# Performance work log

Measured on AMD Instinct MI355X. Metric: run time of the kernel, lower is better.

The kernel has to match this reference:

```python
import jax, jax.numpy as jnp
import numpy as np

B, S, D, H = 4, 1024, 1024, 16
HS = D // H  # head_size = 64


def setup_inputs() -> dict:
    key = jax.random.key(0)
    ks = jax.random.split(key, 12)
    sc_d = 1.0 / np.sqrt(D)
    sc_h = 1.0 / np.sqrt(HS)
    inp = {
        "queries": jax.random.normal(ks[0], (B, S, D), jnp.float32),
        "keys": jax.random.normal(ks[1], (B, S, D), jnp.float32),
        "values": jax.random.normal(ks[2], (B, S, D), jnp.float32),
        # causal mask: scores where mask == 0 are filled with -1e9
        "mask": jnp.tril(jnp.ones((S, S), jnp.int32)),
        # per-head query/key projections: [H, D, HS] weights, [H, HS] biases
        "Wq": jax.random.uniform(ks[3], (H, D, HS), jnp.float32, -sc_d, sc_d),
        "bq": jax.random.uniform(ks[4], (H, HS), jnp.float32, -sc_d, sc_d),
        "Wk": jax.random.uniform(ks[5], (H, D, HS), jnp.float32, -sc_d, sc_d),
        "bk": jax.random.uniform(ks[6], (H, HS), jnp.float32, -sc_d, sc_d),
        # shared value projection: [D, HS]
        "Wv": jax.random.uniform(ks[7], (D, HS), jnp.float32, -sc_d, sc_d),
        "bv": jax.random.uniform(ks[8], (HS,), jnp.float32, -sc_d, sc_d),
        # output projection: [HS, D]
        "Wo": jax.random.uniform(ks[9], (HS, D), jnp.float32, -sc_h, sc_h),
        "bo": jax.random.uniform(ks[10], (D,), jnp.float32, -sc_h, sc_h),
    }
    return inp


def reference(queries, keys, values, mask, Wq, bq, Wk, bk, Wv, bv, Wo, bo):
    # shared value projection: [B, S, HS]
    v = jnp.einsum("bsd,de->bse", values, Wv) + bv
    # batched per-head projections (replaces the python loop over heads)
    q = jnp.einsum("bsd,hde->bhse", queries, Wq) + bq[None, :, None, :]
    k = jnp.einsum("btd,hde->bhte", keys, Wk) + bk[None, :, None, :]
    scores = jnp.einsum("bhse,bhte->bhst", q, k) / jnp.sqrt(jnp.float32(HS))
    scores = jnp.where(mask == 0, jnp.float32(-1e9), scores)
    attn = jax.nn.softmax(scores, axis=-1)  # [B, H, S, S]; dropout = eval-mode identity
    head_out = jnp.einsum("bhst,bte->bhse", attn, v)
    out = head_out.mean(axis=1)  # mean over heads -> [B, S, HS]
    out = jnp.einsum("bse,ed->bsd", out, Wo) + bo
    attention_weights = attn.mean(axis=1)  # [B, S, S]
    return out, attention_weights
```

## Files before the change

### kernel.cpp

```cpp
#include <hip/hip_runtime.h>
#include <hip/hip_bf16.h>
#include <stdint.h>

typedef _Float16 half8 __attribute__((ext_vector_type(8)));
typedef _Float16 half4 __attribute__((ext_vector_type(4)));
typedef float    f32x4 __attribute__((ext_vector_type(4)));

#define MFMA16(a, b, c) __builtin_amdgcn_mfma_f32_16x16x32_f16(a, b, c, 0, 0, 0)

typedef __attribute__((address_space(1))) const void GVOID;
typedef __attribute__((address_space(3))) void LVOID;
__device__ __forceinline__ void glds16(const void* g, void* l)
{
    __builtin_amdgcn_global_load_lds((GVOID*)g, (LVOID*)l, 16, 0, 0);
}

__global__ __launch_bounds__(256) void transpose_to_f16(
    const float* __restrict__ X, _Float16* __restrict__ Y,
    int R, int C, long inBS, long outBS)
{
    __shared__ float t[32][33];
    const int bz = blockIdx.z;
    X += (long)bz * inBS;
    Y += (long)bz * outBS;
    const int c0 = blockIdx.x * 32, r0 = blockIdx.y * 32;
    const int tx = threadIdx.x & 31, ty = threadIdx.x >> 5;
#pragma unroll
    for (int i = 0; i < 4; ++i)
        t[ty + i * 8][tx] = X[(long)(r0 + ty + i * 8) * C + c0 + tx];
    __syncthreads();
#pragma unroll
    for (int i = 0; i < 4; ++i)
        Y[(long)(c0 + ty + i * 8) * R + r0 + tx] = (_Float16)t[tx][ty + i * 8];
}

__global__ __launch_bounds__(256) void cvt_qk_f16(
    const float* __restrict__ S0, const float* __restrict__ S1,
    _Float16* __restrict__ D)
{
    const float* S = blockIdx.y ? S1 : S0;
    _Float16* Dz = D + (long)blockIdx.y * 4194304;
    const long i = ((long)blockIdx.x * 256 + threadIdx.x) * 8;
    const float4 v0 = *(const float4*)(S + i);
    const float4 v1 = *(const float4*)(S + i + 4);
    half8 h;
    h[0] = (_Float16)v0.x; h[1] = (_Float16)v0.y;
    h[2] = (_Float16)v0.z; h[3] = (_Float16)v0.w;
    h[4] = (_Float16)v1.x; h[5] = (_Float16)v1.y;
    h[6] = (_Float16)v1.z; h[7] = (_Float16)v1.w;
    *(half8*)(Dz + i) = h;
}

__global__ __launch_bounds__(256, 2) void gemm_qk_glds(
    const _Float16* __restrict__ A16,
    const _Float16* __restrict__ BT,
    const float* __restrict__ bias0, const float* __restrict__ bias1,
    _Float16* __restrict__ Cout)
{
    __shared__ __align__(16) _Float16 As[2][128 * 64];
    __shared__ __align__(16) _Float16 Bs[2][128 * 64];

    const int gx  = gridDim.x, gy = gridDim.y;
    const int nwg = gx * gy * (int)gridDim.z;
    const int lid = (int)blockIdx.x + gx * ((int)blockIdx.y + gy * (int)blockIdx.z);
    const int q8  = nwg >> 3;
    const int xcd = lid & 7, loc = lid >> 3;
    const int sw  = xcd * q8 + loc;
    const int nt  = sw % gx;
    const int tm2 = sw / gx;
    const int mt  = tm2 % gy;
    const int z   = tm2 / gy;

    const int n0 = nt * 128;
    const int m0 = mt * 128;
    const int tid  = threadIdx.x;
    const int wave = tid >> 6, lane = tid & 63;
    const int m16  = lane & 15, quad = lane >> 4;

    const char* Az = (const char*)(A16 + (long)z * 4194304);
    const char* Bz = (const char*)(BT  + (long)z * 1048576);

    const int colbyte = (((lane & 7) ^ (lane >> 3)) << 4);
    const char* gaBase = Az + ((long)(m0 + wave * 32 + (lane >> 3)) << 11) + colbyte;
    const char* gbBase = Bz + ((long)(n0 + wave * 32 + (lane >> 3)) << 11) + colbyte;

    f32x4 acc[2][8];
    {
        f32x4 zz = {0.f, 0.f, 0.f, 0.f};
#pragma unroll
        for (int i = 0; i < 2; ++i)
#pragma unroll
            for (int j = 0; j < 8; ++j) acc[i][j] = zz;
    }

    auto STAGE = [&](int bf, int k0) {
        const char* ga = gaBase + (k0 << 1);
        const char* gb = gbBase + (k0 << 1);
        _Float16* la = &As[bf][wave * 32 * 64];
        _Float16* lb = &Bs[bf][wave * 32 * 64];
#pragma unroll
        for (int i = 0; i < 4; ++i) {
            glds16(ga + (long)i * 8 * 2048, la + i * 8 * 64);
            glds16(gb + (long)i * 8 * 2048, lb + i * 8 * 64);
        }
    };

    auto COMPUTE = [&](int bf) {
        const char* Ab = (const char*)&As[bf][0];
        const char* Bp = (const char*)&Bs[bf][0];
        const int sw4 = (m16 & 7) << 4;
#pragma unroll
        for (int kss = 0; kss < 2; ++kss) {
            const int kbs = (kss * 64 + quad * 16) ^ sw4;
            const half8 a0 = *(const half8*)(Ab + (wave * 32 + m16) * 128 + kbs);
            const half8 a1 = *(const half8*)(Ab + (wave * 32 + 16 + m16) * 128 + kbs);
#pragma unroll
            for (int c = 0; c < 8; ++c) {
                const half8 bfr = *(const half8*)(Bp + (c * 16 + m16) * 128 + kbs);
                acc[0][c] = MFMA16(a0, bfr, acc[0][c]);
                acc[1][c] = MFMA16(a1, bfr, acc[1][c]);
            }
        }
    };

    STAGE(0, 0);
    __syncthreads();
    int cur = 0;
    for (int k0 = 0; k0 < 1024; k0 += 64) {
        if (k0 + 64 < 1024) STAGE(cur ^ 1, k0 + 64);
        COMPUTE(cur);
        __syncthreads();
        cur ^= 1;
    }

    const float* bias = z ? bias1 : bias0;
    _Float16* Cz = Cout + (long)z * 4194304;
#pragma unroll
    for (int hh = 0; hh < 2; ++hh) {
#pragma unroll
        for (int c = 0; c < 8; ++c) {
            const int col = n0 + c * 16 + m16;
            const float bb = bias[col];
#pragma unroll
            for (int r = 0; r < 4; ++r) {
                const int row = m0 + wave * 32 + hh * 16 + quad * 4 + r;
                Cz[(long)row * 1024 + col] = (_Float16)(acc[hh][c][r] + bb);
            }
        }
    }
}

__global__ __launch_bounds__(256, 2) void gemm_f16_v2(
    const float* __restrict__ A0, const float* __restrict__ A1,
    const _Float16* __restrict__ BT,
    const float* __restrict__ bias0, const float* __restrict__ bias1,
    void* __restrict__ Cout,
    int N, int lda, int ldbt, int ldc,
    long aBS, long bBS, long cBS,
    int c_half, int atomic, int nks, int kchunk)
{
    __shared__ __align__(16) _Float16 As[128][72];
    __shared__ __align__(16) _Float16 Bs[128][72];

    const int gx  = gridDim.x, gy = gridDim.y;
    const int nwg = gx * gy * (int)gridDim.z;
    const int lid = (int)blockIdx.x + gx * ((int)blockIdx.y + gy * (int)blockIdx.z);
    const int q8  = nwg >> 3, r8 = nwg & 7;
    const int xcd = lid & 7, loc = lid >> 3;
    const int sw  = (xcd < r8 ? xcd * (q8 + 1) : r8 * (q8 + 1) + (xcd - r8) * q8) + loc;
    const int nt  = sw % gx;
    const int tm2 = sw / gx;
    const int mt  = tm2 % gy;
    const int bz  = tm2 / gy;

    const int b = bz / nks, ks = bz % nks;
    const int kbeg = ks * kchunk;
    const int kend = kbeg + kchunk;

    const float* A = A1 ? (b ? A1 : A0) : (A0 + (long)b * aBS);
    const _Float16* Bb = BT + (long)b * bBS;

    const int n0 = nt * 128;
    const int m0 = mt * 128;
    const int tid  = threadIdx.x;
    const int wave = tid >> 6, lane = tid & 63;
    const int m16  = lane & 15, quad = lane >> 4;

    const int acol = (tid & 15) * 4;
    const int arb  = tid >> 4;
    const int bj   = tid >> 1;
    const int bcc  = (tid & 1) * 32;
    int jn = n0 + bj; if (jn > N - 1) jn = N - 1;
    const _Float16* bpB = Bb + (long)jn * ldbt;

    f32x4 acc[2][8];
    {
        f32x4 zz = {0.f, 0.f, 0.f, 0.f};
#pragma unroll
        for (int i = 0; i < 2; ++i)
#pragma unroll
            for (int j = 0; j < 8; ++j) acc[i][j] = zz;
    }

    for (int k0 = kbeg; k0 < kend; k0 += 64) {
        {
            const int cc = acol;
            float4 av[8];
#pragma unroll
            for (int p = 0; p < 8; ++p)
                av[p] = *(const float4*)(A + (long)(m0 + arb + p * 16) * lda + k0 + cc);
#pragma unroll
            for (int p = 0; p < 8; ++p) {
                half4 hv;
                hv[0] = (_Float16)av[p].x; hv[1] = (_Float16)av[p].y;
                hv[2] = (_Float16)av[p].z; hv[3] = (_Float16)av[p].w;
                *(half4*)&As[arb + p * 16][cc] = hv;
            }
        }
        {
            const _Float16* bp = bpB + k0 + bcc;
            half8 b0 = *(const half8*)(bp);
            half8 b1 = *(const half8*)(bp + 8);
            half8 b2 = *(const half8*)(bp + 16);
            half8 b3 = *(const half8*)(bp + 24);
            *(half8*)&Bs[bj][bcc]      = b0;
            *(half8*)&Bs[bj][bcc + 8]  = b1;
            *(half8*)&Bs[bj][bcc + 16] = b2;
            *(half8*)&Bs[bj][bcc + 24] = b3;
        }
        __syncthreads();
#pragma unroll
        for (int kss = 0; kss < 2; ++kss) {
            const int ko = kss * 32 + quad * 8;
            const half8 a0 = *(const half8*)&As[wave * 32 + m16][ko];
            const half8 a1 = *(const half8*)&As[wave * 32 + 16 + m16][ko];
#pragma unroll
            for (int c = 0; c < 8; ++c) {
                const half8 bf = *(const half8*)&Bs[c * 16 + m16][ko];
                acc[0][c] = MFMA16(a0, bf, acc[0][c]);
                acc[1][c] = MFMA16(a1, bf, acc[1][c]);
            }
        }
        __syncthreads();
    }

    const float* bias = b ? bias1 : bias0;
    const int addb = (bias != nullptr) && (kbeg == 0);
#pragma unroll
    for (int hh = 0; hh < 2; ++hh) {
#pragma unroll
        for (int c = 0; c < 8; ++c) {
            const int col = n0 + c * 16 + m16;
            if (col >= N) continue;
            const float bb = addb ? bias[col] : 0.f;
#pragma unroll
            for (int r = 0; r < 4; ++r) {
                const int row = m0 + wave * 32 + hh * 16 + quad * 4 + r;
                const float v = acc[hh][c][r] + bb;
                const long idx = (long)b * cBS + (long)row * ldc + col;
                if (atomic)      atomicAdd(&((float*)Cout)[idx], v);
                else if (c_half) ((_Float16*)Cout)[idx] = (_Float16)v;
                else             ((float*)Cout)[idx] = v;
            }
        }
    }
}

__global__ __launch_bounds__(256, 4) void attn_stats(
    const _Float16* __restrict__ q_all, const _Float16* __restrict__ k_all,
    float* __restrict__ m_out, float* __restrict__ il_out)
{
    const int st = blockIdx.x, h = blockIdx.y, b = blockIdx.z;
    const int tid = threadIdx.x, wave = tid >> 6, lane = tid & 63;
    const int m16 = lane & 15, quad = lane >> 4;
    const int s0 = st * 64;
    const int sw = s0 + wave * 16;

    __shared__ __align__(16) _Float16 qs[64][72];
    __shared__ __align__(16) _Float16 ks[64][72];

    const int srow = tid >> 2;
    const int scol = (tid & 3) * 16;

    {
        const _Float16* qsrc = q_all + ((long)(b * 1024 + s0 + srow)) * 1024 + h * 64 + scol;
        *(half8*)&qs[srow][scol]     = *(const half8*)(qsrc);
        *(half8*)&qs[srow][scol + 8] = *(const half8*)(qsrc + 8);
    }

    const _Float16* ksrcb = k_all + ((long)(b * 1024 + srow)) * 1024 + h * 64 + scol;

    float mr[4], lr[4];
#pragma unroll
    for (int r = 0; r < 4; ++r) { mr[r] = -3.0e38f; lr[r] = 0.f; }

    half8 a0, a1;
    for (int tt = 0; tt <= st; ++tt) {
        const _Float16* ksrc = ksrcb + (long)(tt * 64) * 1024;
        const half8 k0 = *(const half8*)(ksrc);
        const half8 k1 = *(const half8*)(ksrc + 8);

        __syncthreads();
        *(half8*)&ks[srow][scol]     = k0;
        *(half8*)&ks[srow][scol + 8] = k1;
        __syncthreads();

        if (tt == 0) {
            a0 = *(const half8*)&qs[wave * 16 + m16][quad * 8];
            a1 = *(const half8*)&qs[wave * 16 + m16][quad * 8 + 32];
        }

        if (tt < st) {
#pragma unroll
            for (int c = 0; c < 4; ++c) {
                const half8 b0 = *(const half8*)&ks[c * 16 + m16][quad * 8];
                const half8 b1 = *(const half8*)&ks[c * 16 + m16][quad * 8 + 32];
                f32x4 cc = {0.f, 0.f, 0.f, 0.f};
                cc = MFMA16(a0, b0, cc);
                cc = MFMA16(a1, b1, cc);
#pragma unroll
                for (int r = 0; r < 4; ++r) {
                    const float zz = cc[r] * 0.125f;
                    const float nm = fmaxf(mr[r], zz);
                    lr[r] = lr[r] * __expf(mr[r] - nm) + __expf(zz - nm);
                    mr[r] = nm;
                }
            }
        } else {
#pragma unroll
            for (int c = 0; c < 4; ++c) {
                const half8 b0 = *(const half8*)&ks[c * 16 + m16][quad * 8];
                const half8 b1 = *(const half8*)&ks[c * 16 + m16][quad * 8 + 32];
                f32x4 cc = {0.f, 0.f, 0.f, 0.f};
                cc = MFMA16(a0, b0, cc);
                cc = MFMA16(a1, b1, cc);
                const int col = tt * 64 + c * 16 + m16;
#pragma unroll
                for (int r = 0; r < 4; ++r) {
                    const int row = sw + quad * 4 + r;
                    if (col <= row) {
                        const float zz = cc[r] * 0.125f;
                        const float nm = fmaxf(mr[r], zz);
                        lr[r] = lr[r] * __expf(mr[r] - nm) + __expf(zz - nm);
                        mr[r] = nm;
                    }
                }
            }
        }
    }

#pragma unroll
    for (int mk = 1; mk < 16; mk <<= 1) {
#pragma unroll
        for (int r = 0; r < 4; ++r) {
            const float om = __shfl_xor(mr[r], mk);
            const float ol = __shfl_xor(lr[r], mk);
            const float nm = fmaxf(mr[r], om);
            lr[r] = lr[r] * __expf(mr[r] - nm) + ol * __expf(om - nm);
            mr[r] = nm;
        }
    }
    if (m16 == 0) {
#pragma unroll
        for (int r = 0; r < 4; ++r) {
            const long idx = ((long)(b * 16 + h)) * 1024 + sw + quad * 4 + r;
            m_out[idx]  = mr[r];
            il_out[idx] = 1.f / lr[r];
        }
    }
}

__global__ __launch_bounds__(256, 4) void attn_pmean(
    const _Float16* __restrict__ q_all, const _Float16* __restrict__ k_all,
    const float* __restrict__ m_in, const float* __restrict__ il_in,
    const _Float16* __restrict__ vT,
    float* __restrict__ attn,
    float* __restrict__ ctx)
{
    const int ttile = blockIdx.x, stile = blockIdx.y, b = blockIdx.z;
    const int tid = threadIdx.x;
    if (ttile > stile) {
        const int c4 = (tid & 15) * 4;
        float4 zz = {0.f, 0.f, 0.f, 0.f};
#pragma unroll
        for (int i = 0; i < 4; ++i) {
            const int r = stile * 64 + (tid >> 4) + i * 16;
            *(float4*)&attn[((long)(b * 1024 + r)) * 1024 + ttile * 64 + c4] = zz;
        }
        return;
    }

    __shared__ __align__(16) _Float16 qs[64][72];
    __shared__ __align__(16) _Float16 ks[64][72];
    __shared__ __align__(16) _Float16 ps[64][72];

    const int wave = tid >> 6, lane = tid & 63;
    const int m16 = lane & 15, quad = lane >> 4;
    const int s0 = stile * 64;
    const int t0 = ttile * 64;
    const int sw = s0 + wave * 16;
    const int diag = (ttile == stile);

    const int srow = tid >> 2;
    const int scol = (tid & 3) * 16;

    const _Float16* qsrc = q_all + ((long)(b * 1024 + s0 + srow)) * 1024 + scol;
    const _Float16* ksrc = k_all + ((long)(b * 1024 + t0 + srow)) * 1024 + scol;
    const long sbase = ((long)(b * 16)) * 1024 + sw + quad * 4;

    float pm[4][4];
#pragma unroll
    for (int c = 0; c < 4; ++c)
#pragma unroll
        for (int r = 0; r < 4; ++r) pm[c][r] = 0.f;

    for (int h = 0; h < 16; ++h) {
        const int ho = h * 64;
        const half8 q0 = *(const half8*)(qsrc + ho);
        const half8 q1 = *(const half8*)(qsrc + ho + 8);
        const half8 k0 = *(const half8*)(ksrc + ho);
        const half8 k1 = *(const half8*)(ksrc + ho + 8);
        const long idx = sbase + (long)h * 1024;
        const float4 mv = *(const float4*)&m_in[idx];
        const float4 iv = *(const float4*)&il_in[idx];

        __syncthreads();
        *(half8*)&qs[srow][scol]     = q0;
        *(half8*)&qs[srow][scol + 8] = q1;
        *(half8*)&ks[srow][scol]     = k0;
        *(half8*)&ks[srow][scol + 8] = k1;
        __syncthreads();

        const half8 a0 = *(const half8*)&qs[wave * 16 + m16][quad * 8];
        const half8 a1 = *(const half8*)&qs[wave * 16 + m16][quad * 8 + 32];
        const float mrow[4] = {mv.x, mv.y, mv.z, mv.w};
        const float irow[4] = {iv.x, iv.y, iv.z, iv.w};

        if (!diag) {
#pragma unroll
            for (int c = 0; c < 4; ++c) {
                const half8 b0 = *(const half8*)&ks[c * 16 + m16][quad * 8];
                const half8 b1 = *(const half8*)&ks[c * 16 + m16][quad * 8 + 32];
                f32x4 cc = {0.f, 0.f, 0.f, 0.f};
                cc = MFMA16(a0, b0, cc);
                cc = MFMA16(a1, b1, cc);
#pragma unroll
                for (int r = 0; r < 4; ++r)
                    pm[c][r] += __expf(cc[r] * 0.125f - mrow[r]) * irow[r];
            }
        } else {
#pragma unroll
            for (int c = 0; c < 4; ++c) {
                const half8 b0 = *(const half8*)&ks[c * 16 + m16][quad * 8];
                const half8 b1 = *(const half8*)&ks[c * 16 + m16][quad * 8 + 32];
                f32x4 cc = {0.f, 0.f, 0.f, 0.f};
                cc = MFMA16(a0, b0, cc);
                cc = MFMA16(a1, b1, cc);
                const int col = t0 + c * 16 + m16;
#pragma unroll
                for (int r = 0; r < 4; ++r) {
                    const int row = sw + quad * 4 + r;
                    if (col <= row)
                        pm[c][r] += __expf(cc[r] * 0.125f - mrow[r]) * irow[r];
                }
            }
        }
    }

#pragma unroll
    for (int c = 0; c < 4; ++c) {
#pragma unroll
        for (int r = 0; r < 4; ++r) {
            const int rloc = (wave << 4) + (quad << 2) + r;
            const int cloc = c * 16 + m16;
            const float p = pm[c][r] * 0.0625f;
            attn[((long)(b * 1024 + s0 + rloc)) * 1024 + t0 + cloc] = p;
            ps[rloc][cloc] = (_Float16)p;
        }
    }
    __syncthreads();

    const _Float16* vTb = vT + (long)b * 65536 + t0;
    f32x4 apv[4];
    {
        f32x4 zz = {0.f, 0.f, 0.f, 0.f};
#pragma unroll
        for (int c = 0; c < 4; ++c) apv[c] = zz;
    }
#pragma unroll
    for (int kss = 0; kss < 2; ++kss) {
        const half8 a = *(const half8*)&ps[wave * 16 + m16][kss * 32 + quad * 8];
#pragma unroll
        for (int c = 0; c < 4; ++c) {
            const half8 bf = *(const half8*)(vTb + (long)(c * 16 + m16) * 1024 + kss * 32 + quad * 8);
            apv[c] = MFMA16(a, bf, apv[c]);
        }
    }
#pragma unroll
    for (int c = 0; c < 4; ++c) {
#pragma unroll
        for (int r = 0; r < 4; ++r) {
            const int row = sw + quad * 4 + r;
            const int e   = c * 16 + m16;
            atomicAdd(&ctx[((long)(b * 1024 + row)) * 64 + e], apv[c][r]);
        }
    }
}

extern "C" void kernel_launch(void* const* d_in, const int* in_sizes, int n_in,
                              void* d_out, int out_size, void* d_ws, size_t ws_size,
                              hipStream_t stream)
{
    const float* queries = (const float*)d_in[0];
    const float* keys    = (const float*)d_in[1];
    const float* values  = (const float*)d_in[2];
    const float* Wq = (const float*)d_in[4];
    const float* bq = (const float*)d_in[5];
    const float* Wk = (const float*)d_in[6];
    const float* bk = (const float*)d_in[7];
    const float* Wv = (const float*)d_in[8];
    const float* bv = (const float*)d_in[9];
    const float* Wo = (const float*)d_in[10];
    const float* bo = (const float*)d_in[11];

    float* out_ptr  = (float*)d_out;
    float* attn_ptr = out_ptr + (long)4096 * 1024;

    uint8_t* w = (uint8_t*)d_ws;
    size_t off = 0;
    auto alloc = [&](size_t bytes) {
        void* p = w + off;
        off = (off + bytes + 255) & ~(size_t)255;
        return p;
    };
    _Float16* WqkT  = (_Float16*)alloc((size_t)2 * 1024 * 1024 * 2);
    _Float16* WvT   = (_Float16*)alloc((size_t)64 * 1024 * 2);
    _Float16* WoT   = (_Float16*)alloc((size_t)1024 * 64 * 2);
    _Float16* qkall = (_Float16*)alloc((size_t)2 * 4194304 * 2);
    _Float16* a16   = (_Float16*)alloc((size_t)2 * 4194304 * 2);
    float*    vbuf  = (float*)alloc((size_t)4096 * 64 * 4);
    _Float16* vT    = (_Float16*)alloc((size_t)4 * 64 * 1024 * 2);
    float*    ctx   = (float*)alloc((size_t)4096 * 64 * 4);
    float*    mbuf  = (float*)alloc((size_t)65536 * 4);
    float*    ilbuf = (float*)alloc((size_t)65536 * 4);
    (void)ws_size; (void)in_sizes; (void)n_in; (void)out_size;

    _Float16* qall = qkall;
    _Float16* kall = qkall + (long)4194304;

    transpose_to_f16<<<dim3(2, 32, 16), 256, 0, stream>>>(Wq, WqkT, 1024, 64, 65536, 65536);
    transpose_to_f16<<<dim3(2, 32, 16), 256, 0, stream>>>(Wk, WqkT + (long)1024 * 1024, 1024, 64, 65536, 65536);
    transpose_to_f16<<<dim3(2, 32, 1),  256, 0, stream>>>(Wv, WvT, 1024, 64, 0, 0);
    transpose_to_f16<<<dim3(32, 2, 1),  256, 0, stream>>>(Wo, WoT, 64, 1024, 0, 0);
    cvt_qk_f16<<<dim3(2048, 2, 1), 256, 0, stream>>>(queries, keys, a16);

    gemm_qk_glds<<<dim3(8, 32, 2), 256, 0, stream>>>(
        a16, WqkT, bq, bk, qkall);

    hipMemsetAsync(vbuf, 0, (size_t)4096 * 64 * 4, stream);
    gemm_f16_v2<<<dim3(1, 32, 8), 256, 0, stream>>>(
        values, nullptr, WvT, bv, nullptr, vbuf,
        64, 1024, 1024, 64,
        0, 0, 0,
        0, 1, 8, 128);

    transpose_to_f16<<<dim3(2, 32, 4), 256, 0, stream>>>(vbuf, vT, 1024, 64, 65536, 65536);

    hipMemsetAsync(ctx, 0, (size_t)4096 * 64 * 4, stream);
    attn_stats<<<dim3(16, 16, 4), 256, 0, stream>>>(qall, kall, mbuf, ilbuf);
    attn_pmean<<<dim3(16, 16, 4), 256, 0, stream>>>(qall, kall, mbuf, ilbuf, vT, attn_ptr, ctx);

    gemm_f16_v2<<<dim3(8, 32, 1), 256, 0, stream>>>(
        ctx, nullptr, WoT, bo, nullptr, out_ptr,
        1024, 64, 64, 1024,
        0, 0, 0,
        0, 0, 1, 64);
}
```

Baseline: 241.8 us.

## Pipeline projection GEMM and attn_pmean with depth-2 async LDS prefetch

The projection GEMM now issues two stages of global-to-LDS loads up front and waits with vmcnt-counted barriers, keeping one tile in flight during compute. attn_pmean replaces its per-head register-staged q/k loads with double-buffered, XOR-swizzled direct global_load_lds copies prefetched two heads ahead. It also preloads all per-head softmax stats into LDS once. The larger LDS footprint lowers the occupancy hint from 4 to 3 blocks, which is a risk if latency hiding relied on more waves.

```diff
diff --git a/kernel.cpp b/kernel.cpp
--- a/kernel.cpp
+++ b/kernel.cpp
@@ -14,6 +14,10 @@
 {
     __builtin_amdgcn_global_load_lds((GVOID*)g, (LVOID*)l, 16, 0, 0);
 }
+
+#define BARRIER() do { asm volatile("" ::: "memory"); \
+    __builtin_amdgcn_s_barrier(); \
+    asm volatile("" ::: "memory"); } while (0)
 
 __global__ __launch_bounds__(256) void transpose_to_f16(
     const float* __restrict__ X, _Float16* __restrict__ Y,
@@ -124,14 +128,21 @@
     };
 
     STAGE(0, 0);
-    __syncthreads();
+    STAGE(1, 64);
     int cur = 0;
-    for (int k0 = 0; k0 < 1024; k0 += 64) {
-        if (k0 + 64 < 1024) STAGE(cur ^ 1, k0 + 64);
+    for (int t = 0; t < 15; ++t) {
+        asm volatile("s_waitcnt vmcnt(8)" ::: "memory");
+        __builtin_amdgcn_sched_barrier(0);
+        BARRIER();
         COMPUTE(cur);
-        __syncthreads();
+        BARRIER();
+        if (t < 14) STAGE(cur, (t + 2) * 64);
         cur ^= 1;
     }
+    asm volatile("s_waitcnt vmcnt(0)" ::: "memory");
+    __builtin_amdgcn_sched_barrier(0);
+    BARRIER();
+    COMPUTE(cur);
 
     const float* bias = z ? bias1 : bias0;
     _Float16* Cz = Cout + (long)z * 4194304;
@@ -204,17 +215,16 @@
 
     for (int k0 = kbeg; k0 < kend; k0 += 64) {
         {
-            const int cc = acol;
             float4 av[8];
 #pragma unroll
             for (int p = 0; p < 8; ++p)
-                av[p] = *(const float4*)(A + (long)(m0 + arb + p * 16) * lda + k0 + cc);
+                av[p] = *(const float4*)(A + (long)(m0 + arb + p * 16) * lda + k0 + acol);
 #pragma unroll
             for (int p = 0; p < 8; ++p) {
                 half4 hv;
                 hv[0] = (_Float16)av[p].x; hv[1] = (_Float16)av[p].y;
                 hv[2] = (_Float16)av[p].z; hv[3] = (_Float16)av[p].w;
-                *(half4*)&As[arb + p * 16][cc] = hv;
+                *(half4*)&As[arb + p * 16][acol] = hv;
             }
         }
         {
@@ -370,7 +380,7 @@
     }
 }
 
-__global__ __launch_bounds__(256, 4) void attn_pmean(
+__global__ __launch_bounds__(256, 3) void attn_pmean(
     const _Float16* __restrict__ q_all, const _Float16* __restrict__ k_all,
     const float* __restrict__ m_in, const float* __restrict__ il_in,
     const _Float16* __restrict__ vT,
@@ -390,9 +400,11 @@
         return;
     }
 
-    __shared__ __align__(16) _Float16 qs[64][72];
-    __shared__ __align__(16) _Float16 ks[64][72];
+    __shared__ __align__(16) _Float16 qs2[2][64 * 64];
+    __shared__ __align__(16) _Float16 ks2[2][64 * 64];
     __shared__ __align__(16) _Float16 ps[64][72];
+    __shared__ __align__(16) float mls[16][64];
+    __shared__ __align__(16) float ils[16][64];
 
     const int wave = tid >> 6, lane = tid & 63;
     const int m16 = lane & 15, quad = lane >> 4;
@@ -401,12 +413,35 @@
     const int sw = s0 + wave * 16;
     const int diag = (ttile == stile);
 
-    const int srow = tid >> 2;
-    const int scol = (tid & 3) * 16;
-
-    const _Float16* qsrc = q_all + ((long)(b * 1024 + s0 + srow)) * 1024 + scol;
-    const _Float16* ksrc = k_all + ((long)(b * 1024 + t0 + srow)) * 1024 + scol;
-    const long sbase = ((long)(b * 16)) * 1024 + sw + quad * 4;
+    {
+        const int hh = tid >> 4;
+        const int c4 = (tid & 15) * 4;
+        const long ix = ((long)(b * 16 + hh)) * 1024 + s0 + c4;
+        const float4 mv4 = *(const float4*)&m_in[ix];
+        const float4 iv4 = *(const float4*)&il_in[ix];
+        *(float4*)&mls[hh][c4] = mv4;
+        *(float4*)&ils[hh][c4] = iv4;
+    }
+
+    const int colb = (((lane & 7) ^ (lane >> 3)) << 4);
+    const char* gq = (const char*)q_all + ((long)(b * 1024 + s0 + wave * 16 + (lane >> 3)) << 11) + colb;
+    const char* gk = (const char*)k_all + ((long)(b * 1024 + t0 + wave * 16 + (lane >> 3)) << 11) + colb;
+
+    auto STAGE_P = [&](int bf, int h) {
+        const char* q = gq + h * 128;
+        const char* k = gk + h * 128;
+        _Float16* lq = &qs2[bf][wave * 16 * 64];
+        _Float16* lk = &ks2[bf][wave * 16 * 64];
+        glds16(q, lq);
+        glds16(q + 8 * 2048, lq + 8 * 64);
+        glds16(k, lk);
+        glds16(k + 8 * 2048, lk + 8 * 64);
+    };
+
+    STAGE_P(0, 0);
+    STAGE_P(1, 1);
+    asm volatile("s_waitcnt lgkmcnt(0)" ::: "memory");
+    BARRIER();
 
     float pm[4][4];
 #pragma unroll
@@ -414,33 +449,23 @@
 #pragma unroll
         for (int r = 0; r < 4; ++r) pm[c][r] = 0.f;
 
-    for (int h = 0; h < 16; ++h) {
-        const int ho = h * 64;
-        const half8 q0 = *(const half8*)(qsrc + ho);
-        const half8 q1 = *(const half8*)(qsrc + ho + 8);
-        const half8 k0 = *(const half8*)(ksrc + ho);
-        const half8 k1 = *(const half8*)(ksrc + ho + 8);
-        const long idx = sbase + (long)h * 1024;
-        const float4 mv = *(const float4*)&m_in[idx];
-        const float4 iv = *(const float4*)&il_in[idx];
-
-        __syncthreads();
-        *(half8*)&qs[srow][scol]     = q0;
-        *(half8*)&qs[srow][scol + 8] = q1;
-        *(half8*)&ks[srow][scol]     = k0;
-        *(half8*)&ks[srow][scol + 8] = k1;
-        __syncthreads();
-
-        const half8 a0 = *(const half8*)&qs[wave * 16 + m16][quad * 8];
-        const half8 a1 = *(const half8*)&qs[wave * 16 + m16][quad * 8 + 32];
+    const int swz = (m16 & 7) << 4;
+    int cur = 0;
+
+    auto COMPUTE_H = [&](int h, int bf) {
+        const char* Qc = (const char*)&qs2[bf][0];
+        const char* Kc = (const char*)&ks2[bf][0];
+        const half8 a0 = *(const half8*)(Qc + (wave * 16 + m16) * 128 + ((quad * 16) ^ swz));
+        const half8 a1 = *(const half8*)(Qc + (wave * 16 + m16) * 128 + ((quad * 16 + 64) ^ swz));
+        const float4 mv = *(const float4*)&mls[h][wave * 16 + quad * 4];
+        const float4 iv = *(const float4*)&ils[h][wave * 16 + quad * 4];
         const float mrow[4] = {mv.x, mv.y, mv.z, mv.w};
         const float irow[4] = {iv.x, iv.y, iv.z, iv.w};
-
         if (!diag) {
 #pragma unroll
             for (int c = 0; c < 4; ++c) {
-                const half8 b0 = *(const half8*)&ks[c * 16 + m16][quad * 8];
-                const half8 b1 = *(const half8*)&ks[c * 16 + m16][quad * 8 + 32];
+                const half8 b0 = *(const half8*)(Kc + (c * 16 + m16) * 128 + ((quad * 16) ^ swz));
+                const half8 b1 = *(const half8*)(Kc + (c * 16 + m16) * 128 + ((quad * 16 + 64) ^ swz));
                 f32x4 cc = {0.f, 0.f, 0.f, 0.f};
                 cc = MFMA16(a0, b0, cc);
                 cc = MFMA16(a1, b1, cc);
@@ -451,8 +476,8 @@
         } else {
 #pragma unroll
             for (int c = 0; c < 4; ++c) {
-                const half8 b0 = *(const half8*)&ks[c * 16 + m16][quad * 8];
-                const half8 b1 = *(const half8*)&ks[c * 16 + m16][quad * 8 + 32];
+                const half8 b0 = *(const half8*)(Kc + (c * 16 + m16) * 128 + ((quad * 16) ^ swz));
+                const half8 b1 = *(const half8*)(Kc + (c * 16 + m16) * 128 + ((quad * 16 + 64) ^ swz));
                 f32x4 cc = {0.f, 0.f, 0.f, 0.f};
                 cc = MFMA16(a0, b0, cc);
                 cc = MFMA16(a1, b1, cc);
@@ -465,7 +490,21 @@
                 }
             }
         }
-    }
+    };
+
+    for (int h = 0; h < 15; ++h) {
+        asm volatile("s_waitcnt vmcnt(4)" ::: "memory");
+        __builtin_amdgcn_sched_barrier(0);
+        BARRIER();
+        COMPUTE_H(h, cur);
+        BARRIER();
+        if (h < 14) STAGE_P(cur, h + 2);
+        cur ^= 1;
+    }
+    asm volatile("s_waitcnt vmcnt(0)" ::: "memory");
+    __builtin_amdgcn_sched_barrier(0);
+    BARRIER();
+    COMPUTE_H(15, cur);
 
 #pragma unroll
     for (int c = 0; c < 4; ++c) {
```

Measured after the change: 241.5 us. No clear change (-0.1%).
